# Kernel optimization log

Hardware: AMD Instinct MI355X
Metric: run time of the kernel (lower is better)

The kernel has to match this reference:

```python
import jax, jax.numpy as jnp
import numpy as np

B = 16384
OBS = 568        # 36 self features + 19 * 28 other-agent features
H = 256          # hidden_dim
SELF_DIM = 36
OTHER_DIM = 28
N_OTHER = (OBS - SELF_DIM) // OTHER_DIM  # 19


def _linear_init(key, fan_in, fan_out):
    # torch nn.Linear default: U(-1/sqrt(fan_in), 1/sqrt(fan_in))
    kw, kb = jax.random.split(key)
    s = 1.0 / np.sqrt(fan_in)
    W = jax.random.uniform(kw, (fan_in, fan_out), jnp.float32, -s, s)
    b = jax.random.uniform(kb, (fan_out,), jnp.float32, -s, s)
    return W, b


def setup_inputs() -> dict:
    key = jax.random.key(0)
    ks = jax.random.split(key, 10)
    x = jax.random.normal(ks[0], (B, OBS), jnp.float32)
    eps = jax.random.normal(ks[1], (B, H), jnp.float32)
    W_mu, b_mu = _linear_init(ks[2], OBS, H)
    W_var, b_var = _linear_init(ks[3], OBS, H)
    W_self, b_self = _linear_init(ks[4], SELF_DIM, H)
    W_other, b_other = _linear_init(ks[5], OTHER_DIM, H)
    W_q, b_q = _linear_init(ks[6], H, H)
    W_k, b_k = _linear_init(ks[7], H, H)
    W_v, b_v = _linear_init(ks[8], 2 * H, H)
    W_a, b_a = _linear_init(ks[9], 2 * H, H)
    return {"x": x, "eps": eps,
            "W_mu": W_mu, "b_mu": b_mu, "W_var": W_var, "b_var": b_var,
            "W_self": W_self, "b_self": b_self, "W_other": W_other, "b_other": b_other,
            "W_q": W_q, "b_q": b_q, "W_k": W_k, "b_k": b_k,
            "W_v": W_v, "b_v": b_v, "W_a": W_a, "b_a": b_a}


def reference(x, eps, W_mu, b_mu, W_var, b_var, W_self, b_self,
              W_other, b_other, W_q, b_q, W_k, b_k, W_v, b_v, W_a, b_a):
    relu = jax.nn.relu
    # VAE reparameterization (detach=False path)
    mu = x @ W_mu + b_mu                                  # [B, H]
    log_var = x @ W_var + b_var                           # [B, H]
    z = eps * jnp.exp(0.5 * log_var) + mu                 # [B, H]

    self_info = x[:, :SELF_DIM]                           # [B, 36]
    agents_info = x[:, SELF_DIM:].reshape(B, N_OTHER, OTHER_DIM)  # [B, N, 28]

    self_em = relu(self_info @ W_self + b_self)           # [B, H]
    other_ems = relu(agents_info @ W_other + b_other)     # [B, N, H]

    q = relu(z @ W_q + b_q)                               # [B, H]
    k = relu(other_ems @ W_k + b_k)                       # [B, N, H]
    v_in = jnp.concatenate(
        [other_ems, jnp.broadcast_to(self_em[:, None, :], (B, N_OTHER, H))], axis=-1)
    v = relu(v_in @ W_v + b_v)                            # [B, N, H]

    scores = jnp.einsum('bh,bnh->bn', q, k) / np.sqrt(H)  # [B, N]
    att_weight = jax.nn.softmax(scores, axis=-1)          # [B, N]
    h = jnp.einsum('bn,bnh->bh', att_weight, v)           # [B, H]

    out = relu(jnp.concatenate([h, self_em], axis=-1) @ W_a + b_a)  # [B, H]
    return out, att_weight[:, None, :]                    # att: [B, 1, N]
```

## Files before the change

### kernel.cpp

```cpp
#include <hip/hip_runtime.h>

typedef __bf16 bf16;
typedef __bf16 bf16x4 __attribute__((ext_vector_type(4)));
typedef __bf16 bf16x8 __attribute__((ext_vector_type(8)));
typedef float  f32x4  __attribute__((ext_vector_type(4)));

#define NB    16384
#define NOBS  568
#define NH    256
#define NAG   19

#define OFF_WT_MU    0u
#define OFF_WT_VAR   294912u
#define OFF_WT_SELF  589824u
#define OFF_WT_OTHER 622592u
#define OFF_WT_Q     638976u
#define OFF_WT_K     770048u
#define OFF_WT_V1    901120u
#define OFF_WT_V2    1032192u
#define OFF_WT_A1    1163264u
#define OFF_WT_A2    1294336u
#define OFF_Z        1425408u
#define OFF_SELF     9814016u
#define OFF_Q        18202624u
#define OFF_SV       26591232u
#define OFF_H        34979840u

static __device__ __forceinline__ unsigned short bfbits(float v) {
  bf16 b = (bf16)v;
  union { bf16 b; unsigned short u; } cvt; cvt.b = b; return cvt.u;
}

static __device__ __forceinline__ void gload16(const bf16* g, bf16* l) {
  __builtin_amdgcn_global_load_lds(
      (const __attribute__((address_space(1))) void*)g,
      (__attribute__((address_space(3))) void*)(void*)l, 16, 0, 0);
}

__global__ __launch_bounds__(256) void wprep(
    const float* __restrict__ Wmu, const float* __restrict__ Wvar,
    const float* __restrict__ Wself, const float* __restrict__ Wother,
    const float* __restrict__ Wq, const float* __restrict__ Wk,
    const float* __restrict__ Wv, const float* __restrict__ Wa, char* wsb)
{
  const float* src; bf16* dst; int K, Kp;
  switch (blockIdx.y) {
    case 0: src = Wmu;        dst = (bf16*)(wsb + OFF_WT_MU);    K = 568; Kp = 576; break;
    case 1: src = Wvar;       dst = (bf16*)(wsb + OFF_WT_VAR);   K = 568; Kp = 576; break;
    case 2: src = Wself;      dst = (bf16*)(wsb + OFF_WT_SELF);  K = 36;  Kp = 64;  break;
    case 3: src = Wother;     dst = (bf16*)(wsb + OFF_WT_OTHER); K = 28;  Kp = 32;  break;
    case 4: src = Wq;         dst = (bf16*)(wsb + OFF_WT_Q);     K = 256; Kp = 256; break;
    case 5: src = Wk;         dst = (bf16*)(wsb + OFF_WT_K);     K = 256; Kp = 256; break;
    case 6: src = Wv;         dst = (bf16*)(wsb + OFF_WT_V1);    K = 256; Kp = 256; break;
    case 7: src = Wv + 65536; dst = (bf16*)(wsb + OFF_WT_V2);    K = 256; Kp = 256; break;
    case 8: src = Wa;         dst = (bf16*)(wsb + OFF_WT_A1);    K = 256; Kp = 256; break;
    default: src = Wa + 65536; dst = (bf16*)(wsb + OFF_WT_A2);   K = 256; Kp = 256; break;
  }
  int total = 256 * Kp;
  for (int i = blockIdx.x * 256 + threadIdx.x; i < total; i += gridDim.x * 256) {
    int n = i & 255, kk = (i >> 8) & 31, ch = i >> 13;
    int k = ch * 32 + kk;
    dst[ch * 8192 + n * 32 + kk] = (k < K) ? (bf16)src[k * 256 + n] : (bf16)0.f;
  }
}

__global__ __launch_bounds__(256, 3) void gemm_zself(
    const float* __restrict__ x,
    const bf16* __restrict__ WtMuC, const bf16* __restrict__ WtVarC,
    const bf16* __restrict__ WtSelfC,
    const float* __restrict__ b_mu, const float* __restrict__ b_var,
    const float* __restrict__ b_self, const float* __restrict__ eps,
    bf16* __restrict__ zout, bf16* __restrict__ selfout)
{
  __shared__ bf16 lA[2][64 * 40];
  __shared__ __align__(16) bf16 lB1[2][128 * 32];
  __shared__ __align__(16) bf16 lB2[2][128 * 32];

  const int tid = threadIdx.x;
  const int wave = tid >> 6;
  const int lane = tid & 63;
  const int quad = lane >> 4;
  const int m = lane & 15;
  const int rowbase = blockIdx.x * 64;
  const int colbase = (blockIdx.y & 1) * 128;
  const bool isZ = blockIdx.y < 2;
  const int nch = isZ ? 18 : 2;
  const bf16* __restrict__ W1 = isZ ? WtMuC : WtSelfC;
  const float* __restrict__ bias = isZ ? b_mu : b_self;

  f32x4 acc[8], accB[8];
  const f32x4 z4 = {0.f, 0.f, 0.f, 0.f};
#pragma unroll
  for (int ct = 0; ct < 8; ++ct) { acc[ct] = z4; accB[ct] = z4; }

  const int ar0 = tid >> 3, afs0 = tid & 7;
  const int ar1 = (tid + 256) >> 3, afs1 = (tid + 256) & 7;

  auto loadA = [&](int kc, int fs, int r, float4& f) {
    int k = kc + fs * 4;
    const float* src = x + (size_t)(rowbase + r) * 568 + k;
    if (k + 4 <= 568) {
      f = *(const float4*)src;
    } else {
      f.x = (k + 0 < 568) ? src[0] : 0.f;
      f.y = (k + 1 < 568) ? src[1] : 0.f;
      f.z = (k + 2 < 568) ? src[2] : 0.f;
      f.w = (k + 3 < 568) ? src[3] : 0.f;
    }
  };
  auto writeA = [&](int buf, int fs, int r, const float4& f) {
    bf16x4 o = {(bf16)f.x, (bf16)f.y, (bf16)f.z, (bf16)f.w};
    *(bf16x4*)(&lA[buf][r * 40 + fs * 4]) = o;
  };
  auto stageB = [&](int buf, int ch) {
    const bf16* s1 = W1 + (size_t)ch * 8192 + colbase * 32 + tid * 8;
    gload16(s1, &lB1[buf][wave * 512]);
    gload16(s1 + 2048, &lB1[buf][2048 + wave * 512]);
    if (isZ) {
      const bf16* s2 = WtVarC + (size_t)ch * 8192 + colbase * 32 + tid * 8;
      gload16(s2, &lB2[buf][wave * 512]);
      gload16(s2 + 2048, &lB2[buf][2048 + wave * 512]);
    }
  };

  {
    float4 f0, f1;
    loadA(0, afs0, ar0, f0);
    loadA(0, afs1, ar1, f1);
    stageB(0, 0);
    writeA(0, afs0, ar0, f0);
    writeA(0, afs1, ar1, f1);
  }
  __syncthreads();

  for (int ch = 0; ch < nch; ++ch) {
    const int cur = ch & 1, nxt = cur ^ 1;
    float4 f0, f1;
    const bool more = (ch + 1 < nch);
    if (more) {
      stageB(nxt, ch + 1);
      loadA((ch + 1) * 32, afs0, ar0, f0);
      loadA((ch + 1) * 32, afs1, ar1, f1);
    }
    bf16x8 afrag = *(const bf16x8*)(&lA[cur][(wave * 16 + m) * 40 + quad * 8]);
#pragma unroll
    for (int ct = 0; ct < 8; ++ct) {
      bf16x8 bfrag = *(const bf16x8*)(&lB1[cur][(ct * 16 + m) * 32 + quad * 8]);
      acc[ct] = __builtin_amdgcn_mfma_f32_16x16x32_bf16(afrag, bfrag, acc[ct], 0, 0, 0);
      if (isZ) {
        bf16x8 b2 = *(const bf16x8*)(&lB2[cur][(ct * 16 + m) * 32 + quad * 8]);
        accB[ct] = __builtin_amdgcn_mfma_f32_16x16x32_bf16(afrag, b2, accB[ct], 0, 0, 0);
      }
    }
    if (more) {
      writeA(nxt, afs0, ar0, f0);
      writeA(nxt, afs1, ar1, f1);
    }
    __syncthreads();
  }

#pragma unroll
  for (int ct = 0; ct < 8; ++ct) {
    const int col = colbase + ct * 16 + m;
    const float bv = bias[col];
#pragma unroll
    for (int r = 0; r < 4; ++r) {
      const size_t row = (size_t)rowbase + wave * 16 + quad * 4 + r;
      float v = acc[ct][r] + bv;
      if (isZ) {
        float lv = accB[ct][r] + b_var[col];
        float zz = eps[row * 256 + col] * __expf(0.5f * lv) + v;
        zout[row * 256 + col] = (bf16)zz;
      } else {
        selfout[row * 256 + col] = (bf16)(v > 0.f ? v : 0.f);
      }
    }
  }
}

__global__ __launch_bounds__(256, 6) void gemm_qsv(
    const bf16* __restrict__ zb, const bf16* __restrict__ selfb,
    const bf16* __restrict__ WtQc, const bf16* __restrict__ WtV2c,
    const float* __restrict__ b_q, const float* __restrict__ b_v,
    bf16* __restrict__ qout, bf16* __restrict__ svout)
{
  __shared__ __align__(16) bf16 lA[2][64 * 32];
  __shared__ __align__(16) bf16 lB[2][128 * 32];

  const int tid = threadIdx.x;
  const int wave = tid >> 6;
  const int lane = tid & 63;
  const int quad = lane >> 4;
  const int m = lane & 15;
  const int rowbase = blockIdx.x * 64;
  const int colbase = (blockIdx.y & 1) * 128;
  const bool isQ = blockIdx.y < 2;
  const bf16* __restrict__ Ap = isQ ? zb : selfb;
  const bf16* __restrict__ Wc = isQ ? WtQc : WtV2c;
  const float* __restrict__ bias = isQ ? b_q : b_v;
  bf16* __restrict__ outp = isQ ? qout : svout;

  f32x4 acc[8];
  const f32x4 z4 = {0.f, 0.f, 0.f, 0.f};
#pragma unroll
  for (int ct = 0; ct < 8; ++ct) acc[ct] = z4;

  const size_t arow = (size_t)(rowbase + (tid >> 2)) * 256 + (tid & 3) * 8;
  const size_t bbase = (size_t)colbase * 32 + (size_t)tid * 8;

  gload16(Ap + arow, &lA[0][wave * 512]);
  gload16(Wc + bbase, &lB[0][wave * 512]);
  gload16(Wc + bbase + 2048, &lB[0][2048 + wave * 512]);
  __syncthreads();

#pragma unroll
  for (int ch = 0; ch < 8; ++ch) {
    const int cur = ch & 1;
    if (ch < 7) {
      const int nxt = cur ^ 1;
      const size_t cof = (size_t)(ch + 1) * 8192;
      gload16(Ap + arow + (ch + 1) * 32, &lA[nxt][wave * 512]);
      gload16(Wc + cof + bbase, &lB[nxt][wave * 512]);
      gload16(Wc + cof + bbase + 2048, &lB[nxt][2048 + wave * 512]);
    }
    bf16x8 afrag = *(const bf16x8*)(&lA[cur][(wave * 16 + m) * 32 + quad * 8]);
#pragma unroll
    for (int ct = 0; ct < 8; ++ct) {
      bf16x8 bfrag = *(const bf16x8*)(&lB[cur][(ct * 16 + m) * 32 + quad * 8]);
      acc[ct] = __builtin_amdgcn_mfma_f32_16x16x32_bf16(afrag, bfrag, acc[ct], 0, 0, 0);
    }
    __syncthreads();
  }

#pragma unroll
  for (int ct = 0; ct < 8; ++ct) {
    const int col = colbase + ct * 16 + m;
    const float bv = bias[col];
#pragma unroll
    for (int r = 0; r < 4; ++r) {
      const size_t row = (size_t)rowbase + wave * 16 + quad * 4 + r;
      float v = acc[ct][r] + bv;
      if (isQ) v = (v > 0.f ? v : 0.f);
      outp[row * 256 + col] = (bf16)v;
    }
  }
}

__global__ __launch_bounds__(256, 4) void gemm_dualA(
    const bf16* __restrict__ A1, const bf16* __restrict__ A2,
    const bf16* __restrict__ Wt1c, const bf16* __restrict__ Wt2c,
    const float* __restrict__ bias, float* __restrict__ outp)
{
  __shared__ __align__(16) bf16 lA[2][64 * 32];
  __shared__ __align__(16) bf16 lB[2][64 * 32];

  const int tid = threadIdx.x;
  const int wave = tid >> 6;
  const int lane = tid & 63;
  const int quad = lane >> 4;
  const int m = lane & 15;
  const int rowbase = blockIdx.x * 64;
  const int colbase = blockIdx.y * 64;

  f32x4 acc[4];
  const f32x4 z4 = {0.f, 0.f, 0.f, 0.f};
#pragma unroll
  for (int ct = 0; ct < 4; ++ct) acc[ct] = z4;

  const size_t arow = (size_t)(rowbase + (tid >> 2)) * 256 + (tid & 3) * 8;
  const size_t bbase = (size_t)colbase * 32 + (size_t)tid * 8;

  auto stageT = [&](int buf, int t) {
    const int ch = t & 7;
    const bf16* Astep = (t < 8) ? A1 : A2;
    const bf16* Wstep = (t < 8) ? Wt1c : Wt2c;
    const size_t cof = (size_t)ch * 8192;
    gload16(Astep + arow + ch * 32, &lA[buf][wave * 512]);
    gload16(Wstep + cof + bbase, &lB[buf][wave * 512]);
  };

  stageT(0, 0);
  __syncthreads();

#pragma unroll
  for (int t = 0; t < 16; ++t) {
    const int cur = t & 1;
    if (t < 15) stageT(cur ^ 1, t + 1);
    bf16x8 afrag = *(const bf16x8*)(&lA[cur][(wave * 16 + m) * 32 + quad * 8]);
#pragma unroll
    for (int ct = 0; ct < 4; ++ct) {
      bf16x8 bfrag = *(const bf16x8*)(&lB[cur][(ct * 16 + m) * 32 + quad * 8]);
      acc[ct] = __builtin_amdgcn_mfma_f32_16x16x32_bf16(afrag, bfrag, acc[ct], 0, 0, 0);
    }
    __syncthreads();
  }

#pragma unroll
  for (int ct = 0; ct < 4; ++ct) {
    const int col = colbase + ct * 16 + m;
    const float bv = bias[col];
#pragma unroll
    for (int r = 0; r < 4; ++r) {
      const size_t row = (size_t)rowbase + wave * 16 + quad * 4 + r;
      float v = acc[ct][r] + bv;
      outp[row * 256 + col] = (v > 0.f ? v : 0.f);
    }
  }
}

__global__ __launch_bounds__(512, 4) void k_fused(
    const float* __restrict__ x, const bf16* __restrict__ qb,
    const bf16* __restrict__ svb,
    const bf16* __restrict__ WtOther, const float* __restrict__ b_other,
    const bf16* __restrict__ WtKc, const float* __restrict__ b_k,
    const bf16* __restrict__ WtVc,
    float* __restrict__ att_out, bf16* __restrict__ hb)
{
  __shared__ bf16 ldsO[80 * 264];
  __shared__ bf16 ldsA1[80 * 40];
  __shared__ bf16 qh16[1024];
  __shared__ bf16 svl16[1024];
  float* spart = (float*)ldsA1;
  float* attl  = (float*)ldsA1 + 320;

  const int tid = threadIdx.x, wave = tid >> 6, lane = tid & 63;
  const int quad = lane >> 4, m = lane & 15;
  const int b0 = blockIdx.x * 4;
  const int kvw = wave & 3;
  const bool isV = wave >= 4;

  ((unsigned*)qh16)[tid]  = ((const unsigned*)(qb  + (size_t)b0 * 256))[tid];
  ((unsigned*)svl16)[tid] = ((const unsigned*)(svb + (size_t)b0 * 256))[tid];
  for (int i = tid; i < 80 * 16; i += 512) {
    int r = i >> 4, kk = (i & 15) * 2;
    int n = r >> 2, bb = r & 3;
    float v0 = 0.f, v1 = 0.f;
    if (n < 19) {
      const float* base = x + (size_t)(b0 + bb) * NOBS + 36 + n * 28;
      if (kk < 28) v0 = base[kk];
      if (kk + 1 < 28) v1 = base[kk + 1];
    }
    unsigned u0 = bfbits(v0), u1 = bfbits(v1);
    *(unsigned*)(ldsA1 + r * 40 + kk) = u0 | (u1 << 16);
  }

  const f32x4 z4 = {0.f, 0.f, 0.f, 0.f};

  const bf16* __restrict__ Bc = isV ? WtVc : WtKc;
  const int cb = (kvw * 64 + m) * 32 + quad * 8;
  bf16x8 bE[4];
#pragma unroll
  for (int c = 0; c < 4; ++c) bE[c] = *(const bf16x8*)(Bc + cb + c * 512);

  __syncthreads();

  {
    float bo[2];
    bf16x8 bfr[2];
#pragma unroll
    for (int c = 0; c < 2; ++c) {
      int col = (2 * wave + c) * 16 + m;
      bo[c] = b_other[col];
      bfr[c] = *(const bf16x8*)(WtOther + col * 32 + quad * 8);
    }
    f32x4 acc1[5][2];
#pragma unroll
    for (int rt = 0; rt < 5; ++rt) {
      bf16x8 a = *(const bf16x8*)(ldsA1 + (rt * 16 + m) * 40 + quad * 8);
#pragma unroll
      for (int c = 0; c < 2; ++c)
        acc1[rt][c] = __builtin_amdgcn_mfma_f32_16x16x32_bf16(a, bfr[c], z4, 0, 0, 0);
    }
#pragma unroll
    for (int rt = 0; rt < 5; ++rt)
#pragma unroll
      for (int c = 0; c < 2; ++c) {
        int col = (2 * wave + c) * 16 + m;
#pragma unroll
        for (int r = 0; r < 4; ++r) {
          float v = acc1[rt][c][r] + bo[c];
          v = v > 0.f ? v : 0.f;
          int rowl = rt * 16 + quad * 4 + r;
          ldsO[rowl * 264 + col] = (bf16)v;
        }
      }
  }
  __syncthreads();

  f32x4 acc[5][4];
#pragma unroll
  for (int rt = 0; rt < 5; ++rt)
#pragma unroll
    for (int c = 0; c < 4; ++c) acc[rt][c] = z4;

  {
#pragma unroll 1
    for (int ch = 0; ch < 8; ch += 2) {
      bf16x8 bO[4];
#pragma unroll
      for (int c = 0; c < 4; ++c)
        bO[c] = *(const bf16x8*)(Bc + (size_t)(ch + 1) * 8192 + cb + c * 512);
      const int kc0 = ch * 32;
#pragma unroll
      for (int rt = 0; rt < 5; ++rt) {
        bf16x8 a = *(const bf16x8*)(ldsO + (rt * 16 + m) * 264 + kc0 + quad * 8);
#pragma unroll
        for (int c = 0; c < 4; ++c)
          acc[rt][c] = __builtin_amdgcn_mfma_f32_16x16x32_bf16(a, bE[c], acc[rt][c], 0, 0, 0);
      }
#pragma unroll
      for (int c = 0; c < 4; ++c)
        bE[c] = *(const bf16x8*)(Bc + (size_t)(ch + 2) * 8192 + cb + c * 512);
      const int kc1 = kc0 + 32;
#pragma unroll
      for (int rt = 0; rt < 5; ++rt) {
        bf16x8 a = *(const bf16x8*)(ldsO + (rt * 16 + m) * 264 + kc1 + quad * 8);
#pragma unroll
        for (int c = 0; c < 4; ++c)
          acc[rt][c] = __builtin_amdgcn_mfma_f32_16x16x32_bf16(a, bO[c], acc[rt][c], 0, 0, 0);
      }
    }
  }

  if (!isV) {
    float qreg[4][4], bkreg[4];
#pragma unroll
    for (int c = 0; c < 4; ++c) {
      int col = (4 * wave + c) * 16 + m;
      bkreg[c] = b_k[col];
#pragma unroll
      for (int r = 0; r < 4; ++r) qreg[c][r] = (float)qh16[r * 256 + col];
    }
#pragma unroll
    for (int rt = 0; rt < 5; ++rt) {
      float part[4] = {0.f, 0.f, 0.f, 0.f};
#pragma unroll
      for (int c = 0; c < 4; ++c) {
#pragma unroll
        for (int r = 0; r < 4; ++r) {
          float kv = acc[rt][c][r] + bkreg[c];
          kv = kv > 0.f ? kv : 0.f;
          part[r] += kv * qreg[c][r];
        }
      }
#pragma unroll
      for (int r = 0; r < 4; ++r) {
        float p = part[r];
        p += __shfl_xor(p, 1, 64);
        p += __shfl_xor(p, 2, 64);
        p += __shfl_xor(p, 4, 64);
        p += __shfl_xor(p, 8, 64);
        if (m == 0) spart[wave * 80 + rt * 16 + quad * 4 + r] = p;
      }
    }
  }
  __syncthreads();

  if (!isV && lane < 32) {
    const int bb = wave, j = lane;
    float s = -1e30f;
    if (j < 19) {
      int row = j * 4 + bb;
      s = (spart[row] + spart[80 + row] + spart[160 + row] + spart[240 + row]) * 0.0625f;
    }
    float mx = s;
#pragma unroll
    for (int off = 16; off >= 1; off >>= 1) mx = fmaxf(mx, __shfl_xor(mx, off, 32));
    float e = (j < 19) ? __expf(s - mx) : 0.f;
    float sum = e;
#pragma unroll
    for (int off = 16; off >= 1; off >>= 1) sum += __shfl_xor(sum, off, 32);
    float inv = 1.f / sum;
    float a = e * inv;
    if (j < 20) attl[j * 4 + bb] = a;
    if (j < 19) att_out[(size_t)(b0 + bb) * 19 + j] = a;
  }
  __syncthreads();

  if (isV) {
    float svreg[4][4];
#pragma unroll
    for (int c = 0; c < 4; ++c) {
      int col = (4 * kvw + c) * 16 + m;
#pragma unroll
      for (int r = 0; r < 4; ++r) svreg[c][r] = (float)svl16[r * 256 + col];
    }
    float hacc[4][4];
#pragma unroll
    for (int c = 0; c < 4; ++c)
#pragma unroll
      for (int r = 0; r < 4; ++r) hacc[c][r] = 0.f;
#pragma unroll
    for (int rt = 0; rt < 5; ++rt) {
      float av[4];
#pragma unroll
      for (int r = 0; r < 4; ++r) av[r] = attl[rt * 16 + quad * 4 + r];
#pragma unroll
      for (int c = 0; c < 4; ++c) {
#pragma unroll
        for (int r = 0; r < 4; ++r) {
          float v = acc[rt][c][r] + svreg[c][r];
          v = v > 0.f ? v : 0.f;
          hacc[c][r] += v * av[r];
        }
      }
    }
#pragma unroll
    for (int c = 0; c < 4; ++c)
#pragma unroll
      for (int r = 0; r < 4; ++r) {
        float h = hacc[c][r];
        h += __shfl_xor(h, 16, 64);
        h += __shfl_xor(h, 32, 64);
        if (quad == 0) qh16[r * 256 + (4 * kvw + c) * 16 + m] = (bf16)h;
      }
  }
  __syncthreads();
  ((unsigned*)(hb + (size_t)b0 * 256))[tid] = ((const unsigned*)qh16)[tid];
}

extern "C" void kernel_launch(void* const* d_in, const int* in_sizes, int n_in,
                              void* d_out, int out_size, void* d_ws, size_t ws_size,
                              hipStream_t stream) {
  (void)in_sizes; (void)n_in; (void)out_size; (void)ws_size;
  const float* x      = (const float*)d_in[0];
  const float* eps    = (const float*)d_in[1];
  const float* W_mu   = (const float*)d_in[2];
  const float* b_mu   = (const float*)d_in[3];
  const float* W_var  = (const float*)d_in[4];
  const float* b_var  = (const float*)d_in[5];
  const float* W_self = (const float*)d_in[6];
  const float* b_self = (const float*)d_in[7];
  const float* W_other= (const float*)d_in[8];
  const float* b_other= (const float*)d_in[9];
  const float* W_q    = (const float*)d_in[10];
  const float* b_q    = (const float*)d_in[11];
  const float* W_k    = (const float*)d_in[12];
  const float* b_k    = (const float*)d_in[13];
  const float* W_v    = (const float*)d_in[14];
  const float* b_v    = (const float*)d_in[15];
  const float* W_a    = (const float*)d_in[16];
  const float* b_a    = (const float*)d_in[17];

  char* wsb = (char*)d_ws;
  bf16* WtMu    = (bf16*)(wsb + OFF_WT_MU);
  bf16* WtVar   = (bf16*)(wsb + OFF_WT_VAR);
  bf16* WtSelf  = (bf16*)(wsb + OFF_WT_SELF);
  bf16* WtOther = (bf16*)(wsb + OFF_WT_OTHER);
  bf16* WtQ     = (bf16*)(wsb + OFF_WT_Q);
  bf16* WtK     = (bf16*)(wsb + OFF_WT_K);
  bf16* WtV1    = (bf16*)(wsb + OFF_WT_V1);
  bf16* WtV2    = (bf16*)(wsb + OFF_WT_V2);
  bf16* WtA1    = (bf16*)(wsb + OFF_WT_A1);
  bf16* WtA2    = (bf16*)(wsb + OFF_WT_A2);
  bf16* zbuf    = (bf16*)(wsb + OFF_Z);
  bf16* selfbuf = (bf16*)(wsb + OFF_SELF);
  bf16* qbuf    = (bf16*)(wsb + OFF_Q);
  bf16* svbuf   = (bf16*)(wsb + OFF_SV);
  bf16* hbuf    = (bf16*)(wsb + OFF_H);

  float* out = (float*)d_out;
  float* att_out = out + (size_t)NB * 256;

  dim3 blk(256);
  wprep<<<dim3(160, 10), blk, 0, stream>>>(W_mu, W_var, W_self, W_other, W_q, W_k, W_v, W_a, wsb);
  gemm_zself<<<dim3(NB / 64, 4), blk, 0, stream>>>(x, WtMu, WtVar, WtSelf,
                                                   b_mu, b_var, b_self, eps, zbuf, selfbuf);
  gemm_qsv<<<dim3(NB / 64, 4), blk, 0, stream>>>(zbuf, selfbuf, WtQ, WtV2,
                                                 b_q, b_v, qbuf, svbuf);
  k_fused<<<NB / 4, dim3(512), 0, stream>>>(x, qbuf, svbuf, WtOther, b_other, WtK, b_k,
                                            WtV1, att_out, hbuf);
  gemm_dualA<<<dim3(NB / 64, 4), blk, 0, stream>>>(hbuf, selfbuf, WtA1, WtA2, b_a, out);
}
```

Before: 310.8 us.

## Load x directly into MFMA A-fragments, drop LDS A staging, raise occupancy

The gemm_zself kernel no longer stages the fp32 x tile through shared memory. Each lane now loads its 8 A-operand values straight from global memory into registers, converts them to bf16, and feeds them to the MFMA. The main loop is unrolled by two over the double-buffered B tiles, and launch bounds are raised to 4 blocks per CU. This removes the LDS writes and reads for A and cuts shared memory use, at the cost of less coalesced global loads (each lane reads 32 bytes from a different row) and more register pressure. The loop now assumes an even chunk count, which holds for both the 18-chunk and 2-chunk paths.

```diff
diff --git a/kernel.cpp b/kernel.cpp
--- a/kernel.cpp
+++ b/kernel.cpp
@@ -64,7 +64,7 @@
   }
 }
 
-__global__ __launch_bounds__(256, 3) void gemm_zself(
+__global__ __launch_bounds__(256, 4) void gemm_zself(
     const float* __restrict__ x,
     const bf16* __restrict__ WtMuC, const bf16* __restrict__ WtVarC,
     const bf16* __restrict__ WtSelfC,
@@ -72,7 +72,6 @@
     const float* __restrict__ b_self, const float* __restrict__ eps,
     bf16* __restrict__ zout, bf16* __restrict__ selfout)
 {
-  __shared__ bf16 lA[2][64 * 40];
   __shared__ __align__(16) bf16 lB1[2][128 * 32];
   __shared__ __align__(16) bf16 lB2[2][128 * 32];
 
@@ -93,25 +92,9 @@
 #pragma unroll
   for (int ct = 0; ct < 8; ++ct) { acc[ct] = z4; accB[ct] = z4; }
 
-  const int ar0 = tid >> 3, afs0 = tid & 7;
-  const int ar1 = (tid + 256) >> 3, afs1 = (tid + 256) & 7;
-
-  auto loadA = [&](int kc, int fs, int r, float4& f) {
-    int k = kc + fs * 4;
-    const float* src = x + (size_t)(rowbase + r) * 568 + k;
-    if (k + 4 <= 568) {
-      f = *(const float4*)src;
-    } else {
-      f.x = (k + 0 < 568) ? src[0] : 0.f;
-      f.y = (k + 1 < 568) ? src[1] : 0.f;
-      f.z = (k + 2 < 568) ? src[2] : 0.f;
-      f.w = (k + 3 < 568) ? src[3] : 0.f;
-    }
-  };
-  auto writeA = [&](int buf, int fs, int r, const float4& f) {
-    bf16x4 o = {(bf16)f.x, (bf16)f.y, (bf16)f.z, (bf16)f.w};
-    *(bf16x4*)(&lA[buf][r * 40 + fs * 4]) = o;
-  };
+  const float* __restrict__ xrow =
+      x + (size_t)(rowbase + wave * 16 + m) * 568 + quad * 8;
+
   auto stageB = [&](int buf, int ch) {
     const bf16* s1 = W1 + (size_t)ch * 8192 + colbase * 32 + tid * 8;
     gload16(s1, &lB1[buf][wave * 512]);
@@ -122,40 +105,51 @@
       gload16(s2 + 2048, &lB2[buf][2048 + wave * 512]);
     }
   };
-
-  {
-    float4 f0, f1;
-    loadA(0, afs0, ar0, f0);
-    loadA(0, afs1, ar1, f1);
-    stageB(0, 0);
-    writeA(0, afs0, ar0, f0);
-    writeA(0, afs1, ar1, f1);
-  }
-  __syncthreads();
-
-  for (int ch = 0; ch < nch; ++ch) {
-    const int cur = ch & 1, nxt = cur ^ 1;
-    float4 f0, f1;
-    const bool more = (ch + 1 < nch);
-    if (more) {
-      stageB(nxt, ch + 1);
-      loadA((ch + 1) * 32, afs0, ar0, f0);
-      loadA((ch + 1) * 32, afs1, ar1, f1);
-    }
-    bf16x8 afrag = *(const bf16x8*)(&lA[cur][(wave * 16 + m) * 40 + quad * 8]);
+  auto loadAx = [&](int ch, float4& g0, float4& g1) {
+    const int k = ch * 32 + quad * 8;
+    if (k + 8 <= 568) {
+      g0 = *(const float4*)(xrow + ch * 32);
+      g1 = *(const float4*)(xrow + ch * 32 + 4);
+    } else {
+      g0 = make_float4(0.f, 0.f, 0.f, 0.f);
+      g1 = make_float4(0.f, 0.f, 0.f, 0.f);
+    }
+  };
+  auto cvtA = [&](const float4& g0, const float4& g1) {
+    bf16x8 a;
+    a[0] = (bf16)g0.x; a[1] = (bf16)g0.y; a[2] = (bf16)g0.z; a[3] = (bf16)g0.w;
+    a[4] = (bf16)g1.x; a[5] = (bf16)g1.y; a[6] = (bf16)g1.z; a[7] = (bf16)g1.w;
+    return a;
+  };
+  auto mfmaStep = [&](int buf, const bf16x8& afrag) {
 #pragma unroll
     for (int ct = 0; ct < 8; ++ct) {
-      bf16x8 bfrag = *(const bf16x8*)(&lB1[cur][(ct * 16 + m) * 32 + quad * 8]);
+      bf16x8 bfrag = *(const bf16x8*)(&lB1[buf][(ct * 16 + m) * 32 + quad * 8]);
       acc[ct] = __builtin_amdgcn_mfma_f32_16x16x32_bf16(afrag, bfrag, acc[ct], 0, 0, 0);
       if (isZ) {
-        bf16x8 b2 = *(const bf16x8*)(&lB2[cur][(ct * 16 + m) * 32 + quad * 8]);
+        bf16x8 b2 = *(const bf16x8*)(&lB2[buf][(ct * 16 + m) * 32 + quad * 8]);
         accB[ct] = __builtin_amdgcn_mfma_f32_16x16x32_bf16(afrag, b2, accB[ct], 0, 0, 0);
       }
     }
+  };
+
+  float4 fa0, fa1;
+  stageB(0, 0);
+  loadAx(0, fa0, fa1);
+  __syncthreads();
+
+  for (int ch = 0; ch < nch; ch += 2) {
+    stageB(1, ch + 1);
+    float4 ga0, ga1;
+    loadAx(ch + 1, ga0, ga1);
+    mfmaStep(0, cvtA(fa0, fa1));
+    __syncthreads();
+    const bool more = (ch + 2 < nch);
     if (more) {
-      writeA(nxt, afs0, ar0, f0);
-      writeA(nxt, afs1, ar1, f1);
-    }
+      stageB(0, ch + 2);
+      loadAx(ch + 2, fa0, fa1);
+    }
+    mfmaStep(1, cvtA(ga0, ga1));
     __syncthreads();
   }
 
```

Result: no change. 311.9 us (+0.4%).
